# Optimization experiments

Measured on AMD Instinct MI355X. Metric: run time of the kernel, lower is better.

Reference implementation:

```python
import jax, jax.numpy as jnp
import numpy as np

E = 64          # num_expert
DIN = 512       # d_input
DOUT = 512      # d_output
T = 131072      # total routed tokens (sum of fwd_expert_count)


def setup_inputs() -> dict:
    key = jax.random.key(0)
    k1, k2, k3 = jax.random.split(key, 3)
    inp = jax.random.normal(k1, (T, DIN), dtype=jnp.float32)
    # FMoELinear params: weight [E, d_out, d_in], bias [E, d_out]
    weight = jax.random.normal(k2, (E, DOUT, DIN), dtype=jnp.float32) * (1.0 / np.sqrt(DIN))
    bias = jax.random.normal(k3, (E, DOUT), dtype=jnp.float32) * 0.01
    # Irregular per-expert token counts summing exactly to T (host-side int64,
    # as in fastmoe where fwd_expert_count lives on CPU and drives dispatch).
    rng = np.random.default_rng(0)
    counts = rng.multinomial(T, np.full(E, 1.0 / E))
    fwd_expert_count = np.asarray(counts, dtype=np.int64)
    return {"inp": inp, "weight": weight, "bias": bias, "fwd_expert_count": fwd_expert_count}


def reference(inp, weight, bias, fwd_expert_count):
    # Grouped GEMM: tokens are sorted by expert; expert e owns rows
    # [offs[e], offs[e+1]).  y_i = x_i @ W_e^T + b_e.
    counts = np.asarray(fwd_expert_count)
    offs = np.concatenate([[0], np.cumsum(counts)])
    outs = []
    for e in range(counts.shape[0]):  # fixed small loop over experts
        xe = inp[int(offs[e]):int(offs[e + 1])]          # [n_e, d_in]
        outs.append(xe @ weight[e].T + bias[e])          # [n_e, d_out]
    return jnp.concatenate(outs, axis=0)                 # [T, d_out]
```

## Files before the change

kernel.cpp:

```cpp
#include <hip/hip_runtime.h>
#include <hip/hip_bf16.h>
#include <stdint.h>

#define NE    64
#define DIN   512
#define DOUT  512
#define TTOK  131072
#define BM    256
#define BN    256
#define BK    32
#define NK    (DIN / BK)
#define TILES_TOTAL (TTOK / BM + NE)
#define NXCD  8
#define TPX   (TILES_TOTAL / NXCD)

typedef __bf16 bf16x8_t __attribute__((ext_vector_type(8)));
typedef float  f32x4_t  __attribute__((ext_vector_type(4)));

#define ABUF(i) ((i) * 32768)
#define BBUF(i) (65536 + (i) * 16384)
#define LDS_BYTES 98304

#define WAITV0() asm volatile("s_waitcnt vmcnt(0)" ::: "memory")
#define SB() __builtin_amdgcn_sched_barrier(0)

#define WBF_OFF 32768

__global__ void setup_tiles(const int* __restrict__ cnt, int* __restrict__ ws) {
    int e = threadIdx.x;
    if (e >= NE) return;
    int off = 0, tbase = 0;
    for (int i = 0; i < e; ++i) {
        int c = cnt[i];
        off += c;
        tbase += (c + (BM - 1)) / BM;
    }
    int c = cnt[e];
    int nt = (c + (BM - 1)) / BM;
    int* tbl = ws + 4;
    for (int t = 0; t < nt; ++t) {
        int idx = tbase + t;
        tbl[4 * idx + 0] = e;
        tbl[4 * idx + 1] = off + t * BM;
        tbl[4 * idx + 2] = off + c;
        tbl[4 * idx + 3] = 0;
    }
    if (e == NE - 1) ws[0] = tbase + nt;
}

__global__ __launch_bounds__(256) void wcvt(const float* __restrict__ w,
                                            __bf16* __restrict__ wbf) {
    const size_t stride = (size_t)gridDim.x * 256;
    size_t i = (size_t)blockIdx.x * 256 + threadIdx.x;
    const size_t n8 = (size_t)NE * DOUT * DIN / 8;
    for (; i < n8; i += stride) {
        f32x4_t a = *(const f32x4_t*)(w + i * 8);
        f32x4_t b = *(const f32x4_t*)(w + i * 8 + 4);
        bf16x8_t h;
#pragma unroll
        for (int j = 0; j < 4; ++j) {
            h[j]     = (__bf16)a[j];
            h[4 + j] = (__bf16)b[j];
        }
        *(bf16x8_t*)(wbf + i * 8) = h;
    }
}

__device__ __forceinline__ void gload16(const void* g, uint8_t* l) {
    __builtin_amdgcn_global_load_lds(
        (const __attribute__((address_space(1))) uint32_t*)g,
        (__attribute__((address_space(3))) uint32_t*)l, 16, 0, 0);
}

__global__ __launch_bounds__(1024) void moe_gemm(
    const float* __restrict__ inp,
    const __bf16* __restrict__ wbf,
    const float* __restrict__ bias,
    const int* __restrict__ ws,
    float* __restrict__ out)
{
    __shared__ __align__(16) uint8_t smem[LDS_BYTES];

    const int bid  = blockIdx.x;
    const int xcd  = bid & (NXCD - 1);
    const int slot = bid >> 3;
    const int tile = xcd * TPX + (slot >> 1);
    const int n0   = (slot & 1) * BN;

    const int ntiles = ws[0];
    if (tile >= ntiles) return;
    const int4 ti = ((const int4*)(ws + 4))[tile];
    const int e = ti.x, row0 = ti.y, row_end = ti.z;

    const int tid  = threadIdx.x;
    const int lane = tid & 63;
    const int wave = tid >> 6;
    const int dr = lane >> 3;
    const int ac = lane & 7;
    const int u  = ac ^ dr;

    const float* asrc[2];
#pragma unroll
    for (int i = 0; i < 2; ++i) {
        int arow = wave * 16 + i * 8 + dr;
        int grow = row0 + arow;
        if (grow > row_end - 1) grow = row_end - 1;
        asrc[i] = inp + (size_t)grow * DIN + (u << 2);
    }
    auto issueA = [&](int t, int buf) {
        uint8_t* dst = smem + ABUF(buf) + wave * 2048;
#pragma unroll
        for (int i = 0; i < 2; ++i)
            gload16(asrc[i] + t * BK, dst + i * 1024);
    };

    const int lr_st = wave * 8 + dr;
    const int dout  = n0 + lr_st + ((u >> 2) << 7);
    const __bf16* bsrc = wbf + (size_t)(e * DOUT + dout) * DIN + (u & 3) * 8;
    auto issueB = [&](int t, int buf) {
        gload16(bsrc + t * BK, smem + BBUF(buf) + wave * 1024);
    };

    const int wr = (wave >> 2) * 64;
    const int wc = (wave & 3) * 64;
    const int frow = lane & 15;
    const int kg   = lane >> 4;

    f32x4_t acc[4][4] = {};

    auto compute = [&](int buf) {
        bf16x8_t af[4], bg[4];
#pragma unroll
        for (int m = 0; m < 4; ++m) {
            const int row = wr + m * 16 + frow;
            const uint8_t* pa = smem + ABUF(buf) + row * 128;
            const int sw = (row & 7) << 4;
            f32x4_t q0 = *(const f32x4_t*)(pa + ((kg * 32)      ^ sw));
            f32x4_t q1 = *(const f32x4_t*)(pa + ((kg * 32 + 16) ^ sw));
#pragma unroll
            for (int j = 0; j < 4; ++j) {
                af[m][j]     = (__bf16)q0[j];
                af[m][4 + j] = (__bf16)q1[j];
            }
        }
#pragma unroll
        for (int n = 0; n < 4; ++n) {
            const int row = wc + n * 16 + frow;
            const int lr  = row & 127;
            const int h   = row >> 7;
            bg[n] = *(const bf16x8_t*)(smem + BBUF(buf) + lr * 128 +
                                       ((h * 64 + kg * 16) ^ ((lr & 7) << 4)));
        }
        __builtin_amdgcn_s_setprio(1);
#pragma unroll
        for (int m = 0; m < 4; ++m)
#pragma unroll
            for (int n = 0; n < 4; ++n)
                acc[m][n] = __builtin_amdgcn_mfma_f32_16x16x32_bf16(
                    af[m], bg[n], acc[m][n], 0, 0, 0);
        __builtin_amdgcn_s_setprio(0);
    };

    issueA(0, 0);
    issueB(0, 0);
    WAITV0(); SB();
    __builtin_amdgcn_s_barrier();
#pragma unroll
    for (int t = 0; t < NK; ++t) {
        const int buf = t & 1;
        if (t + 1 < NK) {
            issueA(t + 1, buf ^ 1);
            issueB(t + 1, buf ^ 1);
        }
        compute(buf);
        if (t + 1 < NK) {
            WAITV0(); SB();
            __builtin_amdgcn_s_barrier();
        }
    }

    const int crow = kg * 4;
    const int ccol = frow;
    float bv[4];
#pragma unroll
    for (int n = 0; n < 4; ++n)
        bv[n] = bias[e * DOUT + n0 + wc + n * 16 + ccol];
#pragma unroll
    for (int m = 0; m < 4; ++m) {
#pragma unroll
        for (int j = 0; j < 4; ++j) {
            const int grow = row0 + wr + m * 16 + crow + j;
            if (grow < row_end) {
                float* orow = out + (size_t)grow * DOUT + n0 + wc + ccol;
#pragma unroll
                for (int n = 0; n < 4; ++n)
                    orow[n * 16] = acc[m][n][j] + bv[n];
            }
        }
    }
}

extern "C" void kernel_launch(void* const* d_in, const int* in_sizes, int n_in,
                              void* d_out, int out_size, void* d_ws, size_t ws_size,
                              hipStream_t stream) {
    const float* inp    = (const float*)d_in[0];
    const float* weight = (const float*)d_in[1];
    const float* bias   = (const float*)d_in[2];
    const int* cnt      = (const int*)d_in[3];
    float* out = (float*)d_out;
    int* ws = (int*)d_ws;
    __bf16* wbf = (__bf16*)((char*)d_ws + WBF_OFF);

    hipLaunchKernelGGL(setup_tiles, dim3(1), dim3(64), 0, stream, cnt, ws);
    hipLaunchKernelGGL(wcvt, dim3(2048), dim3(256), 0, stream, weight, wbf);
    hipLaunchKernelGGL(moe_gemm, dim3(TILES_TOTAL * 2), dim3(1024), 0, stream,
                       inp, wbf, bias, ws, out);
}
```

Measured before the change: 200.0 us.

## Triple-buffer LDS stages with prefetch distance two and interleave A conversion with MFMA

Changes the K loop from double buffering with a full vmcnt(0) wait to a three-stage LDS ring. Global-to-LDS loads are issued two tiles ahead, and a partial vmcnt wait keeps one stage's loads in flight during compute. The compute step now converts each A fragment from fp32 to bf16 just before its MFMA row, rather than converting all four up front, to lower register pressure and overlap conversion with matrix work. LDS use grows to about 144 KB, and a launch-bounds occupancy hint is added.

Result: faster. 183.9 us, median of 2 (-8.0%).

```diff
diff --git a/kernel.cpp b/kernel.cpp
--- a/kernel.cpp
+++ b/kernel.cpp
@@ -9,7 +9,7 @@
 #define BM    256
 #define BN    256
 #define BK    32
-#define NK    (DIN / BK)
+#define NKT   (DIN / BK)
 #define TILES_TOTAL (TTOK / BM + NE)
 #define NXCD  8
 #define TPX   (TILES_TOTAL / NXCD)
@@ -18,11 +18,13 @@
 typedef float  f32x4_t  __attribute__((ext_vector_type(4)));
 
 #define ABUF(i) ((i) * 32768)
-#define BBUF(i) (65536 + (i) * 16384)
-#define LDS_BYTES 98304
-
-#define WAITV0() asm volatile("s_waitcnt vmcnt(0)" ::: "memory")
+#define BBUF(i) (98304 + (i) * 16384)
+#define LDS_BYTES 147456
+
+#define WAITV(n) asm volatile("s_waitcnt vmcnt(" #n ")" ::: "memory")
+#define LGKM0()  asm volatile("s_waitcnt lgkmcnt(0)" ::: "memory")
 #define SB() __builtin_amdgcn_sched_barrier(0)
+#define BAR() __builtin_amdgcn_s_barrier()
 
 #define WBF_OFF 32768
 
@@ -72,7 +74,7 @@
         (__attribute__((address_space(3))) uint32_t*)l, 16, 0, 0);
 }
 
-__global__ __launch_bounds__(1024) void moe_gemm(
+__global__ __launch_bounds__(1024, 2) void moe_gemm(
     const float* __restrict__ inp,
     const __bf16* __restrict__ wbf,
     const float* __restrict__ bias,
@@ -105,20 +107,18 @@
         int arow = wave * 16 + i * 8 + dr;
         int grow = row0 + arow;
         if (grow > row_end - 1) grow = row_end - 1;
-        asrc[i] = inp + (size_t)grow * DIN + (u << 2);
-    }
-    auto issueA = [&](int t, int buf) {
-        uint8_t* dst = smem + ABUF(buf) + wave * 2048;
-#pragma unroll
-        for (int i = 0; i < 2; ++i)
-            gload16(asrc[i] + t * BK, dst + i * 1024);
-    };
-
-    const int lr_st = wave * 8 + dr;
-    const int dout  = n0 + lr_st + ((u >> 2) << 7);
-    const __bf16* bsrc = wbf + (size_t)(e * DOUT + dout) * DIN + (u & 3) * 8;
-    auto issueB = [&](int t, int buf) {
-        gload16(bsrc + t * BK, smem + BBUF(buf) + wave * 1024);
+        asrc[i] = inp + (size_t)grow * DIN + u * 4;
+    }
+    const int blr = wave * 8 + dr;
+    const __bf16* bsrc = wbf + (size_t)(e * DOUT + n0 + blr + ((u >> 2) << 7)) * DIN
+                         + (u & 3) * 8;
+
+    auto issueSet = [&](int tk) {
+        const int s = tk % 3;
+        uint8_t* adst = smem + ABUF(s) + wave * 2048;
+        gload16(asrc[0] + tk * BK, adst);
+        gload16(asrc[1] + tk * BK, adst + 1024);
+        gload16(bsrc + tk * BK, smem + BBUF(s) + wave * 1024);
     };
 
     const int wr = (wave >> 2) * 64;
@@ -128,54 +128,52 @@
 
     f32x4_t acc[4][4] = {};
 
-    auto compute = [&](int buf) {
-        bf16x8_t af[4], bg[4];
-#pragma unroll
-        for (int m = 0; m < 4; ++m) {
-            const int row = wr + m * 16 + frow;
-            const uint8_t* pa = smem + ABUF(buf) + row * 128;
-            const int sw = (row & 7) << 4;
-            f32x4_t q0 = *(const f32x4_t*)(pa + ((kg * 32)      ^ sw));
-            f32x4_t q1 = *(const f32x4_t*)(pa + ((kg * 32 + 16) ^ sw));
-#pragma unroll
-            for (int j = 0; j < 4; ++j) {
-                af[m][j]     = (__bf16)q0[j];
-                af[m][4 + j] = (__bf16)q1[j];
-            }
-        }
+    auto computeTile = [&](int tk) {
+        const int s = tk % 3;
+        bf16x8_t bg[4];
 #pragma unroll
         for (int n = 0; n < 4; ++n) {
             const int row = wc + n * 16 + frow;
             const int lr  = row & 127;
             const int h   = row >> 7;
-            bg[n] = *(const bf16x8_t*)(smem + BBUF(buf) + lr * 128 +
-                                       ((h * 64 + kg * 16) ^ ((lr & 7) << 4)));
-        }
-        __builtin_amdgcn_s_setprio(1);
-#pragma unroll
-        for (int m = 0; m < 4; ++m)
+            bg[n] = *(const bf16x8_t*)(smem + BBUF(s) + lr * 128 +
+                        ((h * 64 + kg * 16) ^ ((lr & 7) << 4)));
+        }
+#pragma unroll
+        for (int q = 0; q < 4; ++q) {
+            const int row = wr + q * 16 + frow;
+            const uint8_t* pa = smem + ABUF(s) + row * 128;
+            const int sw = (row & 7) << 4;
+            f32x4_t q0 = *(const f32x4_t*)(pa + ((kg * 32)      ^ sw));
+            f32x4_t q1 = *(const f32x4_t*)(pa + ((kg * 32 + 16) ^ sw));
+            bf16x8_t af;
+#pragma unroll
+            for (int j = 0; j < 4; ++j) {
+                af[j]     = (__bf16)q0[j];
+                af[4 + j] = (__bf16)q1[j];
+            }
+            __builtin_amdgcn_s_setprio(1);
 #pragma unroll
             for (int n = 0; n < 4; ++n)
-                acc[m][n] = __builtin_amdgcn_mfma_f32_16x16x32_bf16(
-                    af[m], bg[n], acc[m][n], 0, 0, 0);
-        __builtin_amdgcn_s_setprio(0);
+                acc[q][n] = __builtin_amdgcn_mfma_f32_16x16x32_bf16(
+                    af, bg[n], acc[q][n], 0, 0, 0);
+            __builtin_amdgcn_s_setprio(0);
+        }
     };
 
-    issueA(0, 0);
-    issueB(0, 0);
-    WAITV0(); SB();
-    __builtin_amdgcn_s_barrier();
-#pragma unroll
-    for (int t = 0; t < NK; ++t) {
-        const int buf = t & 1;
-        if (t + 1 < NK) {
-            issueA(t + 1, buf ^ 1);
-            issueB(t + 1, buf ^ 1);
-        }
-        compute(buf);
-        if (t + 1 < NK) {
-            WAITV0(); SB();
-            __builtin_amdgcn_s_barrier();
+    issueSet(0); SB();
+    issueSet(1); SB();
+    WAITV(3); SB();
+    BAR();
+
+#pragma unroll
+    for (int t = 0; t < NKT; ++t) {
+        if (t + 2 < NKT) { issueSet(t + 2); SB(); }
+        computeTile(t);
+        if (t + 1 < NKT) {
+            if (t + 2 < NKT) { WAITV(3); } else { WAITV(0); }
+            SB();
+            BAR();
         }
     }
 
```
